# Performance work log

Hardware: AMD Instinct MI355X
Metric: run time of the kernel (lower is better)

## Reference

```python
import jax, jax.numpy as jnp
import numpy as np

K = 16                 # neighbors
CH = (64, 64, 64)      # edge-MLP channels
C_IN = 64              # input feature channels
EPS = 1e-3             # Keras BatchNormalization default epsilon


def setup_inputs() -> dict:
    key = jax.random.key(0)
    ks = jax.random.split(key, 24)
    B, N = 256, 128
    inp = {}
    inp["points"] = jax.random.normal(ks[0], (B, N, 2), jnp.float32)
    inp["features"] = jax.random.normal(ks[1], (B, N, C_IN), jnp.float32)
    ins = [2 * C_IN, CH[0], CH[1]]
    i = 2
    for l, (cin, cout) in enumerate(zip(ins, CH)):
        inp[f"w{l}"] = jax.random.normal(ks[i], (cin, cout), jnp.float32) / np.sqrt(cin).astype(np.float32); i += 1
        inp[f"g{l}"] = jnp.ones((cout,), jnp.float32)
        inp[f"b{l}"] = jnp.zeros((cout,), jnp.float32)
        inp[f"m{l}"] = 0.1 * jax.random.normal(ks[i], (cout,), jnp.float32); i += 1
        inp[f"v{l}"] = jnp.ones((cout,), jnp.float32)
    inp["wsc"] = jax.random.normal(ks[i], (C_IN, CH[-1]), jnp.float32) / np.sqrt(C_IN).astype(np.float32); i += 1
    inp["gsc"] = jnp.ones((CH[-1],), jnp.float32)
    inp["bsc"] = jnp.zeros((CH[-1],), jnp.float32)
    inp["msc"] = 0.1 * jax.random.normal(ks[i], (CH[-1],), jnp.float32)
    inp["vsc"] = jnp.ones((CH[-1],), jnp.float32)
    return inp


def _bn(x, g, b, m, v):
    # inference-mode BatchNorm over last (channel) axis
    return (x - m) * jax.lax.rsqrt(v + EPS) * g + b


def _forward(points, features, params):
    # pairwise squared distances  [B, N, N]
    r = jnp.sum(points * points, axis=-1, keepdims=True)
    d = r - 2.0 * jnp.einsum('bnd,bmd->bnm', points, points) + jnp.swapaxes(r, 1, 2)
    # k+1 nearest (incl. self), drop self  -> [B, N, K]
    _, idx = jax.lax.top_k(-d, K + 1)
    idx = idx[:, :, 1:]
    # gather neighbor features  [B, N, K, C]
    knn = jax.vmap(lambda f, i: f[i])(features, idx)
    center = features[:, :, None, :]
    # edge features: concat(center, neighbor - center)  [B, N, K, 2C]
    x = jnp.concatenate([jnp.broadcast_to(center, knn.shape), knn - center], axis=-1)
    # edge MLP: 1x1 convs == per-edge matmuls
    for (w, g, b, m, v) in params[:-1]:
        x = jax.nn.relu(_bn(jnp.einsum('bnkc,cd->bnkd', x, w), g, b, m, v))
    pooled = jnp.mean(x, axis=2)                      # [B, N, C_out]
    wsc, gsc, bsc, msc, vsc = params[-1]
    sc = _bn(features @ wsc, gsc, bsc, msc, vsc)      # shortcut 1x1 conv + BN
    return jax.nn.relu(sc + pooled)


def reference(points, features,
              w0, g0, b0, m0, v0,
              w1, g1, b1, m1, v1,
              w2, g2, b2, m2, v2,
              wsc, gsc, bsc, msc, vsc):
    params = [(w0, g0, b0, m0, v0), (w1, g1, b1, m1, v1),
              (w2, g2, b2, m2, v2), (wsc, gsc, bsc, msc, vsc)]
    return _forward(points, features, params)
```

## Files before the change

### kernel.cpp

```cpp
#include <hip/hip_runtime.h>
#include <stdint.h>


#define KK 16
#define EPSV 1e-3f
#define SW0 136
#define SW 72

typedef __bf16 bf16x8 __attribute__((ext_vector_type(8)));
typedef float f32x4 __attribute__((ext_vector_type(4)));
union B8 { uint4 u; bf16x8 v; };

__device__ __forceinline__ unsigned int f2ord(float f) {
  unsigned int u = __float_as_uint(f);
  return (u & 0x80000000u) ? ~u : (u | 0x80000000u);
}
__device__ __forceinline__ unsigned int f2b(float f) {
  unsigned int u = __float_as_uint(f);
  return (u + 0x7FFFu + ((u >> 16) & 1u)) >> 16;
}
__device__ __forceinline__ unsigned int pk(float lo, float hi) {
  return f2b(lo) | (f2b(hi) << 16);
}

__global__ __launch_bounds__(256) void knn_kernel(const float* __restrict__ pts,
                                                  int* __restrict__ knn) {
  __shared__ __align__(16) unsigned long long keys[4][128];
  const int wv = threadIdx.x >> 6;
  const int lane = threadIdx.x & 63;
  const int row = blockIdx.x * 4 + wv;
  const int b = row >> 7;
  const int n = row & 127;
  const float* pb = pts + b * 128 * 2;
  const float xn = pb[2 * n], yn = pb[2 * n + 1];
  const float rn = __fadd_rn(__fmul_rn(xn, xn), __fmul_rn(yn, yn));

  unsigned long long key0, key1;
#pragma unroll
  for (int h = 0; h < 2; ++h) {
    const int j = lane + h * 64;
    const float xj = pb[2 * j], yj = pb[2 * j + 1];
    const float rj = __fadd_rn(__fmul_rn(xj, xj), __fmul_rn(yj, yj));
    const float dot = __fadd_rn(__fmul_rn(xn, xj), __fmul_rn(yn, yj));
    const float d = __fadd_rn(__fsub_rn(rn, __fmul_rn(2.0f, dot)), rj);
    unsigned long long k = ((unsigned long long)f2ord(d) << 32) | (unsigned int)j;
    if (h == 0) key0 = k; else key1 = k;
  }
  keys[wv][lane] = key0;
  keys[wv][lane + 64] = key1;
  int c0 = 0, c1 = 0;
#pragma unroll 8
  for (int j = 0; j < 128; j += 2) {
    const ulonglong2 kp = *(const ulonglong2*)&keys[wv][j];
    c0 += (kp.x < key0); c0 += (kp.y < key0);
    c1 += (kp.x < key1); c1 += (kp.y < key1);
  }
  if (c0 >= 1 && c0 <= 16) knn[row * KK + c0 - 1] = lane;
  if (c1 >= 1 && c1 <= 16) knn[row * KK + c1 - 1] = lane + 64;
}

__global__ __launch_bounds__(256, 2) void mlp_kernel(
    const float* __restrict__ feat, const int* __restrict__ knnIdx,
    const float* __restrict__ w0, const float* __restrict__ g0,
    const float* __restrict__ b0, const float* __restrict__ m0,
    const float* __restrict__ v0, const float* __restrict__ w1,
    const float* __restrict__ g1, const float* __restrict__ b1,
    const float* __restrict__ m1, const float* __restrict__ v1,
    const float* __restrict__ w2, const float* __restrict__ g2,
    const float* __restrict__ b2, const float* __restrict__ m2,
    const float* __restrict__ v2, const float* __restrict__ wsc,
    const float* __restrict__ gsc, const float* __restrict__ bsc,
    const float* __restrict__ msc, const float* __restrict__ vsc,
    float* __restrict__ out) {
  __shared__ __align__(16) unsigned short w0T[64 * SW0];
  __shared__ __align__(16) unsigned short w1T[64 * SW];
  __shared__ __align__(16) unsigned short w2T[64 * SW];
  __shared__ __align__(16) unsigned short wscT[64 * SW];
  __shared__ __align__(16) unsigned short X0[4][16 * SW0];
  __shared__ __align__(16) unsigned short CFB[4][16 * SW];

  const int tid = threadIdx.x;
  const int wv = tid >> 6;
  const int lane = tid & 63;
  const int m = lane & 15;
  const int q4 = lane >> 4;

#pragma unroll
  for (int q = 0; q < 8; ++q) {
    const int v = tid + 256 * q;
    const float4 w = ((const float4*)w0)[v];
    const int i = v >> 4, c = (v & 15) << 2;
    w0T[(c + 0) * SW0 + i] = (unsigned short)f2b(w.x);
    w0T[(c + 1) * SW0 + i] = (unsigned short)f2b(w.y);
    w0T[(c + 2) * SW0 + i] = (unsigned short)f2b(w.z);
    w0T[(c + 3) * SW0 + i] = (unsigned short)f2b(w.w);
  }
#pragma unroll
  for (int q = 0; q < 4; ++q) {
    const int v = tid + 256 * q;
    const int i = v >> 4, c = (v & 15) << 2;
    float4 w = ((const float4*)w1)[v];
    w1T[(c + 0) * SW + i] = (unsigned short)f2b(w.x);
    w1T[(c + 1) * SW + i] = (unsigned short)f2b(w.y);
    w1T[(c + 2) * SW + i] = (unsigned short)f2b(w.z);
    w1T[(c + 3) * SW + i] = (unsigned short)f2b(w.w);
    w = ((const float4*)w2)[v];
    w2T[(c + 0) * SW + i] = (unsigned short)f2b(w.x);
    w2T[(c + 1) * SW + i] = (unsigned short)f2b(w.y);
    w2T[(c + 2) * SW + i] = (unsigned short)f2b(w.z);
    w2T[(c + 3) * SW + i] = (unsigned short)f2b(w.w);
    w = ((const float4*)wsc)[v];
    wscT[(c + 0) * SW + i] = (unsigned short)f2b(w.x);
    wscT[(c + 1) * SW + i] = (unsigned short)f2b(w.y);
    wscT[(c + 2) * SW + i] = (unsigned short)f2b(w.z);
    wscT[(c + 3) * SW + i] = (unsigned short)f2b(w.w);
  }

  float s0[4], o0[4], s1[4], o1[4], s2[4], o2[4], ssc[4], osc[4];
#pragma unroll
  for (int nt = 0; nt < 4; ++nt) {
    const int c = nt * 16 + m;
    float s;
    s = g0[c] / sqrtf(v0[c] + EPSV); s0[nt] = s; o0[nt] = b0[c] - m0[c] * s;
    s = g1[c] / sqrtf(v1[c] + EPSV); s1[nt] = s; o1[nt] = b1[c] - m1[c] * s;
    s = g2[c] / sqrtf(v2[c] + EPSV); s2[nt] = s; o2[nt] = b2[c] - m2[c] * s;
    s = gsc[c] / sqrtf(vsc[c] + EPSV); ssc[nt] = s; osc[nt] = bsc[c] - msc[c] * s;
  }

  const int row0 = blockIdx.x * 64 + wv * 16;
  {
    const int r = lane >> 2, p = lane & 3;
    const float4* fr = (const float4*)(feat + (row0 + r) * 64);
    const float4 a = fr[p * 4 + 0], bq = fr[p * 4 + 1];
    const float4 cq = fr[p * 4 + 2], dq = fr[p * 4 + 3];
    uint4 u0, u1;
    u0.x = pk(a.x, a.y); u0.y = pk(a.z, a.w);
    u0.z = pk(bq.x, bq.y); u0.w = pk(bq.z, bq.w);
    u1.x = pk(cq.x, cq.y); u1.y = pk(cq.z, cq.w);
    u1.z = pk(dq.x, dq.y); u1.w = pk(dq.z, dq.w);
    *(uint4*)&CFB[wv][r * SW + p * 16] = u0;
    *(uint4*)&CFB[wv][r * SW + p * 16 + 8] = u1;
  }
  __syncthreads();

  const f32x4 fzero = {0.f, 0.f, 0.f, 0.f};
  f32x4 sacc[4] = {fzero, fzero, fzero, fzero};
#pragma unroll
  for (int t = 0; t < 2; ++t) {
    B8 af; af.u = *(const uint4*)&CFB[wv][m * SW + t * 32 + q4 * 8];
#pragma unroll
    for (int nt = 0; nt < 4; ++nt) {
      B8 bf_; bf_.u = *(const uint4*)&wscT[(nt * 16 + m) * SW + t * 32 + q4 * 8];
      sacc[nt] = __builtin_amdgcn_mfma_f32_16x16x32_bf16(af.v, bf_.v, sacc[nt], 0, 0, 0);
    }
  }
  float scf[4][4];
#pragma unroll
  for (int nt = 0; nt < 4; ++nt)
#pragma unroll
    for (int r = 0; r < 4; ++r)
      scf[nt][r] = fmaf(sacc[nt][r], ssc[nt], osc[nt]);

  const float* featb = feat + (row0 >> 7) * (128 * 64);
  const int kk = lane >> 2, pp = lane & 3;

  for (int qo = 0; qo < 4; ++qo) {
#pragma unroll
    for (int ri = 0; ri < 4; ++ri) {
      const int rr = qo * 4 + ri;
      const int row = row0 + rr;

      {
        const int j = knnIdx[row * KK + kk];
        const float4* np_ = (const float4*)(featb + j * 64);
        const float4* cp_ = (const float4*)(feat + row * 64);
        const float4 n0 = np_[pp * 4 + 0], n1 = np_[pp * 4 + 1];
        const float4 n2 = np_[pp * 4 + 2], n3 = np_[pp * 4 + 3];
        const float4 c0 = cp_[pp * 4 + 0], c1 = cp_[pp * 4 + 1];
        const float4 c2 = cp_[pp * 4 + 2], c3 = cp_[pp * 4 + 3];
        uint4 u;
        u.x = pk(c0.x, c0.y); u.y = pk(c0.z, c0.w);
        u.z = pk(c1.x, c1.y); u.w = pk(c1.z, c1.w);
        *(uint4*)&X0[wv][kk * SW0 + pp * 16] = u;
        u.x = pk(c2.x, c2.y); u.y = pk(c2.z, c2.w);
        u.z = pk(c3.x, c3.y); u.w = pk(c3.z, c3.w);
        *(uint4*)&X0[wv][kk * SW0 + pp * 16 + 8] = u;
        u.x = pk(n0.x - c0.x, n0.y - c0.y); u.y = pk(n0.z - c0.z, n0.w - c0.w);
        u.z = pk(n1.x - c1.x, n1.y - c1.y); u.w = pk(n1.z - c1.z, n1.w - c1.w);
        *(uint4*)&X0[wv][kk * SW0 + 64 + pp * 16] = u;
        u.x = pk(n2.x - c2.x, n2.y - c2.y); u.y = pk(n2.z - c2.z, n2.w - c2.w);
        u.z = pk(n3.x - c3.x, n3.y - c3.y); u.w = pk(n3.z - c3.z, n3.w - c3.w);
        *(uint4*)&X0[wv][kk * SW0 + 64 + pp * 16 + 8] = u;
      }

      f32x4 acc[4] = {fzero, fzero, fzero, fzero};
#pragma unroll
      for (int t = 0; t < 4; ++t) {
        B8 af; af.u = *(const uint4*)&X0[wv][m * SW0 + t * 32 + q4 * 8];
#pragma unroll
        for (int nt = 0; nt < 4; ++nt) {
          B8 bf_; bf_.u = *(const uint4*)&w0T[(nt * 16 + m) * SW0 + t * 32 + q4 * 8];
          acc[nt] = __builtin_amdgcn_mfma_f32_16x16x32_bf16(af.v, bf_.v, acc[nt], 0, 0, 0);
        }
      }
#pragma unroll
      for (int nt = 0; nt < 4; ++nt)
#pragma unroll
        for (int r2 = 0; r2 < 4; ++r2) {
          const float y = fmaxf(fmaf(acc[nt][r2], s0[nt], o0[nt]), 0.f);
          X0[wv][(q4 * 4 + r2) * SW0 + nt * 16 + m] = (unsigned short)f2b(y);
        }

      acc[0] = fzero; acc[1] = fzero; acc[2] = fzero; acc[3] = fzero;
#pragma unroll
      for (int t = 0; t < 2; ++t) {
        B8 af; af.u = *(const uint4*)&X0[wv][m * SW0 + t * 32 + q4 * 8];
#pragma unroll
        for (int nt = 0; nt < 4; ++nt) {
          B8 bf_; bf_.u = *(const uint4*)&w1T[(nt * 16 + m) * SW + t * 32 + q4 * 8];
          acc[nt] = __builtin_amdgcn_mfma_f32_16x16x32_bf16(af.v, bf_.v, acc[nt], 0, 0, 0);
        }
      }
#pragma unroll
      for (int nt = 0; nt < 4; ++nt)
#pragma unroll
        for (int r2 = 0; r2 < 4; ++r2) {
          const float y = fmaxf(fmaf(acc[nt][r2], s1[nt], o1[nt]), 0.f);
          X0[wv][(q4 * 4 + r2) * SW0 + nt * 16 + m] = (unsigned short)f2b(y);
        }

      acc[0] = fzero; acc[1] = fzero; acc[2] = fzero; acc[3] = fzero;
#pragma unroll
      for (int t = 0; t < 2; ++t) {
        B8 af; af.u = *(const uint4*)&X0[wv][m * SW0 + t * 32 + q4 * 8];
#pragma unroll
        for (int nt = 0; nt < 4; ++nt) {
          B8 bf_; bf_.u = *(const uint4*)&w2T[(nt * 16 + m) * SW + t * 32 + q4 * 8];
          acc[nt] = __builtin_amdgcn_mfma_f32_16x16x32_bf16(af.v, bf_.v, acc[nt], 0, 0, 0);
        }
      }

      float pool[4];
#pragma unroll
      for (int nt = 0; nt < 4; ++nt) {
        float p_ = 0.f;
#pragma unroll
        for (int r2 = 0; r2 < 4; ++r2)
          p_ += fmaxf(fmaf(acc[nt][r2], s2[nt], o2[nt]), 0.f);
        p_ += __shfl_xor(p_, 16);
        p_ += __shfl_xor(p_, 32);
        pool[nt] = p_ * 0.0625f;
      }
      if (q4 == qo) {
#pragma unroll
        for (int nt = 0; nt < 4; ++nt)
          out[row * 64 + nt * 16 + m] = fmaxf(scf[nt][ri] + pool[nt], 0.f);
      }
    }
  }
}

extern "C" void kernel_launch(void* const* d_in, const int* in_sizes, int n_in,
                              void* d_out, int out_size, void* d_ws, size_t ws_size,
                              hipStream_t stream) {
  const float* pts = (const float*)d_in[0];
  const float* feat = (const float*)d_in[1];
  const float* w0 = (const float*)d_in[2];
  const float* g0 = (const float*)d_in[3];
  const float* b0 = (const float*)d_in[4];
  const float* m0 = (const float*)d_in[5];
  const float* v0 = (const float*)d_in[6];
  const float* w1 = (const float*)d_in[7];
  const float* g1 = (const float*)d_in[8];
  const float* b1 = (const float*)d_in[9];
  const float* m1 = (const float*)d_in[10];
  const float* v1 = (const float*)d_in[11];
  const float* w2 = (const float*)d_in[12];
  const float* g2 = (const float*)d_in[13];
  const float* b2 = (const float*)d_in[14];
  const float* m2 = (const float*)d_in[15];
  const float* v2 = (const float*)d_in[16];
  const float* wsc = (const float*)d_in[17];
  const float* gsc = (const float*)d_in[18];
  const float* bsc = (const float*)d_in[19];
  const float* msc = (const float*)d_in[20];
  const float* vsc = (const float*)d_in[21];
  float* out = (float*)d_out;

  int* knn = (int*)d_ws;

  knn_kernel<<<dim3(256 * 128 / 4), dim3(256), 0, stream>>>(pts, knn);
  mlp_kernel<<<dim3(512), dim3(256), 0, stream>>>(
      feat, knn, w0, g0, b0, m0, v0, w1, g1, b1, m1, v1, w2, g2, b2, m2, v2,
      wsc, gsc, bsc, msc, vsc, out);
}
```

Measured before the change: 178.1 us.

## Fuse kNN into MLP kernel, fold BN into weights, split center-term matmul

Merges the separate kNN kernel into the MLP kernel, so each wave computes top-16 neighbours for its 8 rows into LDS as byte indices. This removes the workspace round-trip and one launch. BN scales are folded into the bf16 weights, and the layer-0 center half of the matmul is computed once per row instead of per edge, halving the K dimension of the first per-edge MFMA. LDS is reused across phases, w2 fragments are kept in registers, and the grid doubles to 1024 blocks with an occupancy hint of 3. Folding the scales into bf16 weights slightly changes rounding.

```diff
diff --git a/kernel.cpp b/kernel.cpp
--- a/kernel.cpp
+++ b/kernel.cpp
@@ -1,66 +1,42 @@
 #include <hip/hip_runtime.h>
+#include <hip/hip_bf16.h>
 #include <stdint.h>
 
 
-#define KK 16
 #define EPSV 1e-3f
-#define SW0 136
-#define SW 72
+#define ST 72
 
 typedef __bf16 bf16x8 __attribute__((ext_vector_type(8)));
 typedef float f32x4 __attribute__((ext_vector_type(4)));
 union B8 { uint4 u; bf16x8 v; };
 
-__device__ __forceinline__ unsigned int f2ord(float f) {
-  unsigned int u = __float_as_uint(f);
+__device__ __forceinline__ unsigned f2ord(float f) {
+  unsigned u = __float_as_uint(f);
   return (u & 0x80000000u) ? ~u : (u | 0x80000000u);
 }
-__device__ __forceinline__ unsigned int f2b(float f) {
-  unsigned int u = __float_as_uint(f);
-  return (u + 0x7FFFu + ((u >> 16) & 1u)) >> 16;
-}
-__device__ __forceinline__ unsigned int pk(float lo, float hi) {
-  return f2b(lo) | (f2b(hi) << 16);
-}
-
-__global__ __launch_bounds__(256) void knn_kernel(const float* __restrict__ pts,
-                                                  int* __restrict__ knn) {
-  __shared__ __align__(16) unsigned long long keys[4][128];
-  const int wv = threadIdx.x >> 6;
-  const int lane = threadIdx.x & 63;
-  const int row = blockIdx.x * 4 + wv;
-  const int b = row >> 7;
-  const int n = row & 127;
-  const float* pb = pts + b * 128 * 2;
-  const float xn = pb[2 * n], yn = pb[2 * n + 1];
-  const float rn = __fadd_rn(__fmul_rn(xn, xn), __fmul_rn(yn, yn));
-
-  unsigned long long key0, key1;
-#pragma unroll
-  for (int h = 0; h < 2; ++h) {
-    const int j = lane + h * 64;
-    const float xj = pb[2 * j], yj = pb[2 * j + 1];
-    const float rj = __fadd_rn(__fmul_rn(xj, xj), __fmul_rn(yj, yj));
-    const float dot = __fadd_rn(__fmul_rn(xn, xj), __fmul_rn(yn, yj));
-    const float d = __fadd_rn(__fsub_rn(rn, __fmul_rn(2.0f, dot)), rj);
-    unsigned long long k = ((unsigned long long)f2ord(d) << 32) | (unsigned int)j;
-    if (h == 0) key0 = k; else key1 = k;
-  }
-  keys[wv][lane] = key0;
-  keys[wv][lane + 64] = key1;
-  int c0 = 0, c1 = 0;
-#pragma unroll 8
-  for (int j = 0; j < 128; j += 2) {
-    const ulonglong2 kp = *(const ulonglong2*)&keys[wv][j];
-    c0 += (kp.x < key0); c0 += (kp.y < key0);
-    c1 += (kp.x < key1); c1 += (kp.y < key1);
-  }
-  if (c0 >= 1 && c0 <= 16) knn[row * KK + c0 - 1] = lane;
-  if (c1 >= 1 && c1 <= 16) knn[row * KK + c1 - 1] = lane + 64;
-}
-
-__global__ __launch_bounds__(256, 2) void mlp_kernel(
-    const float* __restrict__ feat, const int* __restrict__ knnIdx,
+__device__ __forceinline__ unsigned short bf1(float x) {
+  union { __hip_bfloat16 h; unsigned short u; } cv;
+  cv.h = __float2bfloat16(x);
+  return cv.u;
+}
+__device__ __forceinline__ unsigned pk2(float lo, float hi) {
+  union { __hip_bfloat162 h; unsigned u; } cv;
+  cv.h = __float22bfloat162_rn(float2{lo, hi});
+  return cv.u;
+}
+__device__ __forceinline__ float r2of(float x, float y) {
+#pragma clang fp contract(off)
+  return __fadd_rn(__fmul_rn(x, x), __fmul_rn(y, y));
+}
+__device__ __forceinline__ float sqdist(float rn, float xn, float yn,
+                                        float xc, float yc, float rc) {
+#pragma clang fp contract(off)
+  const float dot = __fadd_rn(__fmul_rn(xn, xc), __fmul_rn(yn, yc));
+  return __fadd_rn(__fsub_rn(rn, __fmul_rn(2.0f, dot)), rc);
+}
+
+__global__ __launch_bounds__(256, 3) void fused_kernel(
+    const float* __restrict__ pts, const float* __restrict__ feat,
     const float* __restrict__ w0, const float* __restrict__ g0,
     const float* __restrict__ b0, const float* __restrict__ m0,
     const float* __restrict__ v0, const float* __restrict__ w1,
@@ -72,12 +48,13 @@
     const float* __restrict__ gsc, const float* __restrict__ bsc,
     const float* __restrict__ msc, const float* __restrict__ vsc,
     float* __restrict__ out) {
-  __shared__ __align__(16) unsigned short w0T[64 * SW0];
-  __shared__ __align__(16) unsigned short w1T[64 * SW];
-  __shared__ __align__(16) unsigned short w2T[64 * SW];
-  __shared__ __align__(16) unsigned short wscT[64 * SW];
-  __shared__ __align__(16) unsigned short X0[4][16 * SW0];
-  __shared__ __align__(16) unsigned short CFB[4][16 * SW];
+  __shared__ __align__(16) unsigned short w0dT[64 * ST];
+  __shared__ __align__(16) unsigned short w1T[64 * ST];
+  __shared__ __align__(16) char U[32768];
+
+  unsigned short* w0cT = (unsigned short*)U;
+  unsigned short* w2T = (unsigned short*)(U + 8192);
+  unsigned short* wscT = (unsigned short*)(U + 16384);
 
   const int tid = threadIdx.x;
   const int wv = tid >> 6;
@@ -85,171 +62,259 @@
   const int m = lane & 15;
   const int q4 = lane >> 4;
 
+  unsigned short* CFB = (unsigned short*)(U + 24576) + wv * (16 * 64);
+
 #pragma unroll
   for (int q = 0; q < 8; ++q) {
     const int v = tid + 256 * q;
+    const int i = v >> 4;
+    const int c = (v & 15) << 2;
     const float4 w = ((const float4*)w0)[v];
-    const int i = v >> 4, c = (v & 15) << 2;
-    w0T[(c + 0) * SW0 + i] = (unsigned short)f2b(w.x);
-    w0T[(c + 1) * SW0 + i] = (unsigned short)f2b(w.y);
-    w0T[(c + 2) * SW0 + i] = (unsigned short)f2b(w.z);
-    w0T[(c + 3) * SW0 + i] = (unsigned short)f2b(w.w);
+    float s[4];
+#pragma unroll
+    for (int cc = 0; cc < 4; ++cc) s[cc] = g0[c + cc] / sqrtf(v0[c + cc] + EPSV);
+    if (i < 64) {
+      w0cT[(c + 0) * 64 + i] = bf1(w.x * s[0]);
+      w0cT[(c + 1) * 64 + i] = bf1(w.y * s[1]);
+      w0cT[(c + 2) * 64 + i] = bf1(w.z * s[2]);
+      w0cT[(c + 3) * 64 + i] = bf1(w.w * s[3]);
+    } else {
+      const int i2 = i - 64;
+      w0dT[(c + 0) * ST + i2] = bf1(w.x * s[0]);
+      w0dT[(c + 1) * ST + i2] = bf1(w.y * s[1]);
+      w0dT[(c + 2) * ST + i2] = bf1(w.z * s[2]);
+      w0dT[(c + 3) * ST + i2] = bf1(w.w * s[3]);
+    }
   }
 #pragma unroll
   for (int q = 0; q < 4; ++q) {
     const int v = tid + 256 * q;
-    const int i = v >> 4, c = (v & 15) << 2;
-    float4 w = ((const float4*)w1)[v];
-    w1T[(c + 0) * SW + i] = (unsigned short)f2b(w.x);
-    w1T[(c + 1) * SW + i] = (unsigned short)f2b(w.y);
-    w1T[(c + 2) * SW + i] = (unsigned short)f2b(w.z);
-    w1T[(c + 3) * SW + i] = (unsigned short)f2b(w.w);
-    w = ((const float4*)w2)[v];
-    w2T[(c + 0) * SW + i] = (unsigned short)f2b(w.x);
-    w2T[(c + 1) * SW + i] = (unsigned short)f2b(w.y);
-    w2T[(c + 2) * SW + i] = (unsigned short)f2b(w.z);
-    w2T[(c + 3) * SW + i] = (unsigned short)f2b(w.w);
-    w = ((const float4*)wsc)[v];
-    wscT[(c + 0) * SW + i] = (unsigned short)f2b(w.x);
-    wscT[(c + 1) * SW + i] = (unsigned short)f2b(w.y);
-    wscT[(c + 2) * SW + i] = (unsigned short)f2b(w.z);
-    wscT[(c + 3) * SW + i] = (unsigned short)f2b(w.w);
-  }
-
-  float s0[4], o0[4], s1[4], o1[4], s2[4], o2[4], ssc[4], osc[4];
+    const int i = v >> 4;
+    const int c = (v & 15) << 2;
+    {
+      const float4 w = ((const float4*)w1)[v];
+#pragma unroll
+      for (int cc = 0; cc < 4; ++cc) {
+        const float s = g1[c + cc] / sqrtf(v1[c + cc] + EPSV);
+        const float val = (cc == 0 ? w.x : cc == 1 ? w.y : cc == 2 ? w.z : w.w);
+        w1T[(c + cc) * ST + i] = bf1(val * s);
+      }
+    }
+    {
+      const float4 w = ((const float4*)w2)[v];
+#pragma unroll
+      for (int cc = 0; cc < 4; ++cc) {
+        const float s = g2[c + cc] / sqrtf(v2[c + cc] + EPSV);
+        const float val = (cc == 0 ? w.x : cc == 1 ? w.y : cc == 2 ? w.z : w.w);
+        w2T[(c + cc) * 64 + i] = bf1(val * s);
+      }
+    }
+    {
+      const float4 w = ((const float4*)wsc)[v];
+#pragma unroll
+      for (int cc = 0; cc < 4; ++cc) {
+        const float s = gsc[c + cc] / sqrtf(vsc[c + cc] + EPSV);
+        const float val = (cc == 0 ? w.x : cc == 1 ? w.y : cc == 2 ? w.z : w.w);
+        wscT[(c + cc) * 64 + i] = bf1(val * s);
+      }
+    }
+  }
+
+  f32x4 o1vv[4];
+#pragma unroll
+  for (int nt = 0; nt < 4; ++nt)
+#pragma unroll
+    for (int r = 0; r < 4; ++r) {
+      const int c = nt * 16 + q4 * 4 + r;
+      const float s = g1[c] / sqrtf(v1[c] + EPSV);
+      o1vv[nt][r] = b1[c] - m1[c] * s;
+    }
+  float o0s[4], o2s[4], oscs[4];
 #pragma unroll
   for (int nt = 0; nt < 4; ++nt) {
     const int c = nt * 16 + m;
-    float s;
-    s = g0[c] / sqrtf(v0[c] + EPSV); s0[nt] = s; o0[nt] = b0[c] - m0[c] * s;
-    s = g1[c] / sqrtf(v1[c] + EPSV); s1[nt] = s; o1[nt] = b1[c] - m1[c] * s;
-    s = g2[c] / sqrtf(v2[c] + EPSV); s2[nt] = s; o2[nt] = b2[c] - m2[c] * s;
-    s = gsc[c] / sqrtf(vsc[c] + EPSV); ssc[nt] = s; osc[nt] = bsc[c] - msc[c] * s;
-  }
-
-  const int row0 = blockIdx.x * 64 + wv * 16;
+    o0s[nt] = b0[c] - m0[c] * (g0[c] / sqrtf(v0[c] + EPSV));
+    o2s[nt] = b2[c] - m2[c] * (g2[c] / sqrtf(v2[c] + EPSV));
+    oscs[nt] = bsc[c] - msc[c] * (gsc[c] / sqrtf(vsc[c] + EPSV));
+  }
+  __syncthreads();
+
+  const int row0 = blockIdx.x * 32 + wv * 8;
+  const int bb = row0 >> 7;
+  const float* featb = feat + bb * (128 * 64);
+
   {
-    const int r = lane >> 2, p = lane & 3;
+    const int r = lane >> 3, p = lane & 7;
     const float4* fr = (const float4*)(feat + (row0 + r) * 64);
-    const float4 a = fr[p * 4 + 0], bq = fr[p * 4 + 1];
-    const float4 cq = fr[p * 4 + 2], dq = fr[p * 4 + 3];
-    uint4 u0, u1;
-    u0.x = pk(a.x, a.y); u0.y = pk(a.z, a.w);
-    u0.z = pk(bq.x, bq.y); u0.w = pk(bq.z, bq.w);
-    u1.x = pk(cq.x, cq.y); u1.y = pk(cq.z, cq.w);
-    u1.z = pk(dq.x, dq.y); u1.w = pk(dq.z, dq.w);
-    *(uint4*)&CFB[wv][r * SW + p * 16] = u0;
-    *(uint4*)&CFB[wv][r * SW + p * 16 + 8] = u1;
-  }
+    const float4 a = fr[p * 2 + 0], bq = fr[p * 2 + 1];
+    uint4 u{pk2(a.x, a.y), pk2(a.z, a.w), pk2(bq.x, bq.y), pk2(bq.z, bq.w)};
+    *(uint4*)&CFB[r * 64 + p * 8] = u;
+    *(uint4*)&CFB[512 + lane * 8] = make_uint4(0u, 0u, 0u, 0u);
+  }
+
+  B8 w2f[4][2];
+#pragma unroll
+  for (int nt = 0; nt < 4; ++nt)
+#pragma unroll
+    for (int t = 0; t < 2; ++t)
+      w2f[nt][t].u = *(const uint4*)&w2T[(nt * 16 + m) * 64 + t * 32 + q4 * 8];
+
+  const f32x4 fzero = {0.f, 0.f, 0.f, 0.f};
+  f32x4 cacc[4] = {fzero, fzero, fzero, fzero};
+  f32x4 scf[4] = {fzero, fzero, fzero, fzero};
+#pragma unroll
+  for (int t = 0; t < 2; ++t) {
+    B8 af;
+    af.u = *(const uint4*)&CFB[m * 64 + t * 32 + q4 * 8];
+#pragma unroll
+    for (int nt = 0; nt < 4; ++nt) {
+      B8 bf_;
+      bf_.u = *(const uint4*)&w0cT[(nt * 16 + m) * 64 + t * 32 + q4 * 8];
+      cacc[nt] = __builtin_amdgcn_mfma_f32_16x16x32_bf16(af.v, bf_.v, cacc[nt], 0, 0, 0);
+      bf_.u = *(const uint4*)&wscT[(nt * 16 + m) * 64 + t * 32 + q4 * 8];
+      scf[nt] = __builtin_amdgcn_mfma_f32_16x16x32_bf16(af.v, bf_.v, scf[nt], 0, 0, 0);
+    }
+  }
+#pragma unroll
+  for (int nt = 0; nt < 4; ++nt)
+#pragma unroll
+    for (int r = 0; r < 4; ++r) scf[nt][r] += oscs[nt];
+
   __syncthreads();
 
-  const f32x4 fzero = {0.f, 0.f, 0.f, 0.f};
-  f32x4 sacc[4] = {fzero, fzero, fzero, fzero};
-#pragma unroll
-  for (int t = 0; t < 2; ++t) {
-    B8 af; af.u = *(const uint4*)&CFB[wv][m * SW + t * 32 + q4 * 8];
-#pragma unroll
-    for (int nt = 0; nt < 4; ++nt) {
-      B8 bf_; bf_.u = *(const uint4*)&wscT[(nt * 16 + m) * SW + t * 32 + q4 * 8];
-      sacc[nt] = __builtin_amdgcn_mfma_f32_16x16x32_bf16(af.v, bf_.v, sacc[nt], 0, 0, 0);
-    }
-  }
-  float scf[4][4];
+  char* pwb = U + wv * 8192;
+  unsigned short* X = (unsigned short*)pwb;
+  float* cLS = (float*)(pwb + 2304);
+  unsigned char* knnL = (unsigned char*)(pwb + 2304 + 4096);
+
 #pragma unroll
   for (int nt = 0; nt < 4; ++nt)
 #pragma unroll
     for (int r = 0; r < 4; ++r)
-      scf[nt][r] = fmaf(sacc[nt][r], ssc[nt], osc[nt]);
-
-  const float* featb = feat + (row0 >> 7) * (128 * 64);
+      cLS[(q4 * 4 + r) * 64 + nt * 16 + m] = cacc[nt][r] + o0s[nt];
+
+  {
+    unsigned long long* keysW = (unsigned long long*)pwb;
+    const float* pb = pts + bb * 256;
+    const float xa = pb[2 * lane], ya = pb[2 * lane + 1];
+    const float xb2 = pb[2 * lane + 128], yb2 = pb[2 * lane + 129];
+    const float ra = r2of(xa, ya);
+    const float rb = r2of(xb2, yb2);
+    const int nbase = row0 & 127;
+    for (int rr = 0; rr < 8; ++rr) {
+      const int n = nbase + rr;
+      const float xn = pb[2 * n], yn = pb[2 * n + 1];
+      const float rn = r2of(xn, yn);
+      const float d0 = sqdist(rn, xn, yn, xa, ya, ra);
+      const float d1 = sqdist(rn, xn, yn, xb2, yb2, rb);
+      const unsigned long long key0 =
+          ((unsigned long long)f2ord(d0) << 32) | (unsigned)lane;
+      const unsigned long long key1 =
+          ((unsigned long long)f2ord(d1) << 32) | (unsigned)(lane + 64);
+      keysW[lane] = key0;
+      keysW[lane + 64] = key1;
+      int c0 = 0, c1 = 0;
+#pragma unroll 8
+      for (int j = 0; j < 128; j += 2) {
+        const ulonglong2 kp = *(const ulonglong2*)&keysW[j];
+        c0 += (kp.x < key0); c0 += (kp.y < key0);
+        c1 += (kp.x < key1); c1 += (kp.y < key1);
+      }
+      if (c0 >= 1 && c0 <= 16) knnL[rr * 16 + c0 - 1] = (unsigned char)lane;
+      if (c1 >= 1 && c1 <= 16) knnL[rr * 16 + c1 - 1] = (unsigned char)(lane + 64);
+    }
+  }
+
   const int kk = lane >> 2, pp = lane & 3;
-
-  for (int qo = 0; qo < 4; ++qo) {
+  int jv[8];
+#pragma unroll
+  for (int rr = 0; rr < 8; ++rr) jv[rr] = knnL[rr * 16 + kk];
+
+  for (int qo = 0; qo < 2; ++qo) {
 #pragma unroll
     for (int ri = 0; ri < 4; ++ri) {
       const int rr = qo * 4 + ri;
       const int row = row0 + rr;
 
       {
-        const int j = knnIdx[row * KK + kk];
-        const float4* np_ = (const float4*)(featb + j * 64);
+        const float4* np_ = (const float4*)(featb + jv[rr] * 64);
         const float4* cp_ = (const float4*)(feat + row * 64);
         const float4 n0 = np_[pp * 4 + 0], n1 = np_[pp * 4 + 1];
         const float4 n2 = np_[pp * 4 + 2], n3 = np_[pp * 4 + 3];
         const float4 c0 = cp_[pp * 4 + 0], c1 = cp_[pp * 4 + 1];
         const float4 c2 = cp_[pp * 4 + 2], c3 = cp_[pp * 4 + 3];
         uint4 u;
-        u.x = pk(c0.x, c0.y); u.y = pk(c0.z, c0.w);
-        u.z = pk(c1.x, c1.y); u.w = pk(c1.z, c1.w);
-        *(uint4*)&X0[wv][kk * SW0 + pp * 16] = u;
-        u.x = pk(c2.x, c2.y); u.y = pk(c2.z, c2.w);
-        u.z = pk(c3.x, c3.y); u.w = pk(c3.z, c3.w);
-        *(uint4*)&X0[wv][kk * SW0 + pp * 16 + 8] = u;
-        u.x = pk(n0.x - c0.x, n0.y - c0.y); u.y = pk(n0.z - c0.z, n0.w - c0.w);
-        u.z = pk(n1.x - c1.x, n1.y - c1.y); u.w = pk(n1.z - c1.z, n1.w - c1.w);
-        *(uint4*)&X0[wv][kk * SW0 + 64 + pp * 16] = u;
-        u.x = pk(n2.x - c2.x, n2.y - c2.y); u.y = pk(n2.z - c2.z, n2.w - c2.w);
-        u.z = pk(n3.x - c3.x, n3.y - c3.y); u.w = pk(n3.z - c3.z, n3.w - c3.w);
-        *(uint4*)&X0[wv][kk * SW0 + 64 + pp * 16 + 8] = u;
-      }
-
-      f32x4 acc[4] = {fzero, fzero, fzero, fzero};
-#pragma unroll
-      for (int t = 0; t < 4; ++t) {
-        B8 af; af.u = *(const uint4*)&X0[wv][m * SW0 + t * 32 + q4 * 8];
+        u.x = pk2(n0.x - c0.x, n0.y - c0.y); u.y = pk2(n0.z - c0.z, n0.w - c0.w);
+        u.z = pk2(n1.x - c1.x, n1.y - c1.y); u.w = pk2(n1.z - c1.z, n1.w - c1.w);
+        *(uint4*)&X[kk * ST + pp * 16] = u;
+        u.x = pk2(n2.x - c2.x, n2.y - c2.y); u.y = pk2(n2.z - c2.z, n2.w - c2.w);
+        u.z = pk2(n3.x - c3.x, n3.y - c3.y); u.w = pk2(n3.z - c3.z, n3.w - c3.w);
+        *(uint4*)&X[kk * ST + pp * 16 + 8] = u;
+      }
+
+      f32x4 acc[4];
+#pragma unroll
+      for (int nt = 0; nt < 4; ++nt)
+        acc[nt] = *(const f32x4*)&cLS[rr * 64 + nt * 16 + q4 * 4];
+#pragma unroll
+      for (int t = 0; t < 2; ++t) {
+        B8 bf_;
+        bf_.u = *(const uint4*)&X[m * ST + t * 32 + q4 * 8];
 #pragma unroll
         for (int nt = 0; nt < 4; ++nt) {
-          B8 bf_; bf_.u = *(const uint4*)&w0T[(nt * 16 + m) * SW0 + t * 32 + q4 * 8];
+          B8 af;
+          af.u = *(const uint4*)&w0dT[(nt * 16 + m) * ST + t * 32 + q4 * 8];
           acc[nt] = __builtin_amdgcn_mfma_f32_16x16x32_bf16(af.v, bf_.v, acc[nt], 0, 0, 0);
         }
       }
 #pragma unroll
-      for (int nt = 0; nt < 4; ++nt)
-#pragma unroll
-        for (int r2 = 0; r2 < 4; ++r2) {
-          const float y = fmaxf(fmaf(acc[nt][r2], s0[nt], o0[nt]), 0.f);
-          X0[wv][(q4 * 4 + r2) * SW0 + nt * 16 + m] = (unsigned short)f2b(y);
-        }
-
-      acc[0] = fzero; acc[1] = fzero; acc[2] = fzero; acc[3] = fzero;
+      for (int nt = 0; nt < 4; ++nt) {
+        uint2 wq;
+        wq.x = pk2(fmaxf(acc[nt][0], 0.f), fmaxf(acc[nt][1], 0.f));
+        wq.y = pk2(fmaxf(acc[nt][2], 0.f), fmaxf(acc[nt][3], 0.f));
+        *(uint2*)&X[m * ST + nt * 16 + q4 * 4] = wq;
+      }
+
+#pragma unroll
+      for (int nt = 0; nt < 4; ++nt) acc[nt] = o1vv[nt];
 #pragma unroll
       for (int t = 0; t < 2; ++t) {
-        B8 af; af.u = *(const uint4*)&X0[wv][m * SW0 + t * 32 + q4 * 8];
+        B8 bf_;
+        bf_.u = *(const uint4*)&X[m * ST + t * 32 + q4 * 8];
 #pragma unroll
         for (int nt = 0; nt < 4; ++nt) {
-          B8 bf_; bf_.u = *(const uint4*)&w1T[(nt * 16 + m) * SW + t * 32 + q4 * 8];
+          B8 af;
+          af.u = *(const uint4*)&w1T[(nt * 16 + m) * ST + t * 32 + q4 * 8];
           acc[nt] = __builtin_amdgcn_mfma_f32_16x16x32_bf16(af.v, bf_.v, acc[nt], 0, 0, 0);
         }
       }
 #pragma unroll
-      for (int nt = 0; nt < 4; ++nt)
-#pragma unroll
-        for (int r2 = 0; r2 < 4; ++r2) {
-          const float y = fmaxf(fmaf(acc[nt][r2], s1[nt], o1[nt]), 0.f);
-          X0[wv][(q4 * 4 + r2) * SW0 + nt * 16 + m] = (unsigned short)f2b(y);
-        }
-
-      acc[0] = fzero; acc[1] = fzero; acc[2] = fzero; acc[3] = fzero;
+      for (int nt = 0; nt < 4; ++nt) {
+        uint2 wq;
+        wq.x = pk2(fmaxf(acc[nt][0], 0.f), fmaxf(acc[nt][1], 0.f));
+        wq.y = pk2(fmaxf(acc[nt][2], 0.f), fmaxf(acc[nt][3], 0.f));
+        *(uint2*)&X[m * ST + nt * 16 + q4 * 4] = wq;
+      }
+
+#pragma unroll
+      for (int nt = 0; nt < 4; ++nt) acc[nt] = fzero;
 #pragma unroll
       for (int t = 0; t < 2; ++t) {
-        B8 af; af.u = *(const uint4*)&X0[wv][m * SW0 + t * 32 + q4 * 8];
-#pragma unroll
-        for (int nt = 0; nt < 4; ++nt) {
-          B8 bf_; bf_.u = *(const uint4*)&w2T[(nt * 16 + m) * SW + t * 32 + q4 * 8];
-          acc[nt] = __builtin_amdgcn_mfma_f32_16x16x32_bf16(af.v, bf_.v, acc[nt], 0, 0, 0);
-        }
+        B8 af;
+        af.u = *(const uint4*)&X[m * ST + t * 32 + q4 * 8];
+#pragma unroll
+        for (int nt = 0; nt < 4; ++nt)
+          acc[nt] = __builtin_amdgcn_mfma_f32_16x16x32_bf16(af.v, w2f[nt][t].v, acc[nt], 0, 0, 0);
       }
 
       float pool[4];
 #pragma unroll
       for (int nt = 0; nt < 4; ++nt) {
-        float p_ = 0.f;
-#pragma unroll
-        for (int r2 = 0; r2 < 4; ++r2)
-          p_ += fmaxf(fmaf(acc[nt][r2], s2[nt], o2[nt]), 0.f);
-        p_ += __shfl_xor(p_, 16);
-        p_ += __shfl_xor(p_, 32);
-        pool[nt] = p_ * 0.0625f;
+        float p = fmaxf(acc[nt][0] + o2s[nt], 0.f) + fmaxf(acc[nt][1] + o2s[nt], 0.f) +
+                  fmaxf(acc[nt][2] + o2s[nt], 0.f) + fmaxf(acc[nt][3] + o2s[nt], 0.f);
+        p += __shfl_xor(p, 16);
+        p += __shfl_xor(p, 32);
+        pool[nt] = p * 0.0625f;
       }
       if (q4 == qo) {
 #pragma unroll
@@ -287,10 +352,7 @@
   const float* vsc = (const float*)d_in[21];
   float* out = (float*)d_out;
 
-  int* knn = (int*)d_ws;
-
-  knn_kernel<<<dim3(256 * 128 / 4), dim3(256), 0, stream>>>(pts, knn);
-  mlp_kernel<<<dim3(512), dim3(256), 0, stream>>>(
-      feat, knn, w0, g0, b0, m0, v0, w1, g1, b1, m1, v1, w2, g2, b2, m2, v2,
+  fused_kernel<<<dim3(1024), dim3(256), 0, stream>>>(
+      pts, feat, w0, g0, b0, m0, v0, w1, g1, b1, m1, v1, w2, g2, b2, m2, v2,
       wsc, gsc, bsc, msc, vsc, out);
 }
```

New measurement: 208.3 us. 1.17x slower.
